# Kernel tuning notes

Measured on AMD Instinct MI355X. Metric: run time of the kernel, lower is better.

Reference implementation:

```python
import jax, jax.numpy as jnp
import numpy as np
from jax import lax

STRIDE = 4
SCALES = (32.0, 64.0, 128.0)
RATIOS = (0.5, 1.0, 2.0)
PRE_NMS = 6000          # pre_nms_top_n['testing']
POST_NMS = 1000         # post_nms_top_n['testing']
NMS_THRESH = 0.7
MIN_SIZE = 1.0


def make_anchors(fh, fw):
    # 9 base anchors per cell (3 scales x 3 ratios), xyxy centered at cell centers.
    base = []
    for s in SCALES:
        for r in RATIOS:
            w = s * np.sqrt(1.0 / r)
            h = s * np.sqrt(r)
            base.append([-w / 2, -h / 2, w / 2, h / 2])
    base = np.asarray(base, np.float32)                      # [9,4]
    xs = (np.arange(fw, dtype=np.float32) + 0.5) * STRIDE
    ys = (np.arange(fh, dtype=np.float32) + 0.5) * STRIDE
    cx, cy = np.meshgrid(xs, ys)                             # [fh,fw]
    shifts = np.stack([cx, cy, cx, cy], -1)[:, :, None, :]   # [fh,fw,1,4]
    return jnp.asarray((shifts + base[None, None]).reshape(-1, 4))  # [fh*fw*9,4]


def conv(x, w, b):
    y = lax.conv_general_dilated(x, w, (1, 1), 'SAME',
                                 dimension_numbers=('NCHW', 'OIHW', 'NCHW'))
    return y + b[None, :, None, None]


def decode(anchors, deltas):
    wa = anchors[:, 2] - anchors[:, 0]
    ha = anchors[:, 3] - anchors[:, 1]
    cxa = anchors[:, 0] + 0.5 * wa
    cya = anchors[:, 1] + 0.5 * ha
    cx = deltas[:, 0] * wa + cxa
    cy = deltas[:, 1] * ha + cya
    w = jnp.exp(deltas[:, 2]) * wa
    h = jnp.exp(deltas[:, 3]) * ha
    return jnp.stack([cx - 0.5 * w, cy - 0.5 * h, cx + 0.5 * w, cy + 0.5 * h], -1)


def pairwise_iou(a, b):
    area_a = (a[:, 2] - a[:, 0]) * (a[:, 3] - a[:, 1])
    area_b = (b[:, 2] - b[:, 0]) * (b[:, 3] - b[:, 1])
    lt = jnp.maximum(a[:, None, :2], b[None, :, :2])
    rb = jnp.minimum(a[:, None, 2:], b[None, :, 2:])
    wh = jnp.clip(rb - lt, 0.0)
    inter = wh[..., 0] * wh[..., 1]
    return inter / (area_a[:, None] + area_b[None, :] - inter + 1e-9)


def nms_keep(boxes, valid, thresh):
    # boxes already sorted by score descending; greedy suppression.
    n = boxes.shape[0]
    iou = pairwise_iou(boxes, boxes)  # [n,n]
    def body(i, keep):
        suppressed = jnp.any((iou[i] > thresh) & keep)
        return keep.at[i].set(valid[i] & ~suppressed)
    return lax.fori_loop(0, n, body, jnp.zeros(n, bool))


def rpn_forward(feature, w1, b1, w_cls, b_cls, w_reg, b_reg, image_h, image_w,
                detach_for_proposal=True):
    fh, fw = feature.shape[2], feature.shape[3]
    x = jax.nn.relu(conv(feature, w1, b1))
    conf = conv(x, w_cls, b_cls).transpose(0, 2, 3, 1).reshape(-1)        # [N]
    offsets = conv(x, w_reg, b_reg).transpose(0, 2, 3, 1).reshape(-1, 4)  # [N,4]
    if detach_for_proposal:  # original detaches before create_proposal
        conf = lax.stop_gradient(conf)
        offsets = lax.stop_gradient(offsets)
    anchors = make_anchors(fh, fw)

    pre_n = min(PRE_NMS, conf.shape[0])
    scores, idx = lax.top_k(conf, pre_n)
    props = decode(anchors[idx], offsets[idx])
    # process_box: clip to image, drop boxes smaller than min_size (mask form)
    props = jnp.stack([jnp.clip(props[:, 0], 0.0, float(image_w)),
                       jnp.clip(props[:, 1], 0.0, float(image_h)),
                       jnp.clip(props[:, 2], 0.0, float(image_w)),
                       jnp.clip(props[:, 3], 0.0, float(image_h))], -1)
    valid = ((props[:, 2] - props[:, 0]) >= MIN_SIZE) & \
            ((props[:, 3] - props[:, 1]) >= MIN_SIZE)

    keep = nms_keep(lax.stop_gradient(props), valid, NMS_THRESH)
    # compact first POST_NMS kept boxes into a fixed-shape output (zero padded)
    rank = jnp.cumsum(keep) - 1
    dest = jnp.where(keep & (rank < POST_NMS), rank, POST_NMS)
    out = jnp.zeros((POST_NMS + 1, 4), props.dtype).at[dest].set(props)[:POST_NMS]
    return out


def setup_inputs() -> dict:
    key = jax.random.key(0)
    ks = jax.random.split(key, 4)
    return {
        'feature': jax.random.normal(ks[0], (1, 256, 200, 272), jnp.float32),
        'w1': jax.random.normal(ks[1], (256, 256, 3, 3), jnp.float32) * 0.02,
        'b1': jnp.zeros((256,), jnp.float32),
        'w_cls': jax.random.normal(ks[2], (9, 256, 1, 1), jnp.float32) * 0.02,
        'b_cls': jnp.zeros((9,), jnp.float32),
        'w_reg': jax.random.normal(ks[3], (36, 256, 1, 1), jnp.float32) * 0.01,
        'b_reg': jnp.zeros((36,), jnp.float32),
        'image_h': 800,
        'image_w': 1088,
    }


def reference(feature, w1, b1, w_cls, b_cls, w_reg, b_reg, image_h, image_w):
    return rpn_forward(feature, w1, b1, w_cls, b_cls, w_reg, b_reg,
                       image_h, image_w, detach_for_proposal=True)
```

## Files before the change

kernel.cpp:

```cpp
#include <hip/hip_runtime.h>
#include <hip/hip_bf16.h>
#include <math.h>

#define H_ 200
#define W_ 272
#define C_ 256
#define HW 54400
#define NANCH 489600
#define PRE_N 6000
#define POST_N 1000
#define NWORDS 94
#define CHUNK_W 2720
#define SELCAP 16384

#define X_OFF       0ull
#define CONF_OFF    55705600ull
#define HIST1_OFF   57664000ull
#define SEL_OFF     57926144ull
#define SCAL_OFF    58188288ull
#define TOPIDX_OFF  58254080ull
#define BOXES_OFF   58278080ull
#define VALID_OFF   58374080ull
#define MASK_OFF    58398080ull
#define WCR_OFF     65269376ull

__device__ __forceinline__ unsigned fkey(float fv) {
    unsigned u = __float_as_uint(fv);
    return (u & 0x80000000u) ? ~u : (u | 0x80000000u);
}

__global__ __launch_bounds__(256) void k_repack(const float* __restrict__ w1,
                                                float* __restrict__ w1r) {
    int d = blockIdx.x * 256 + threadIdx.x;
    int o = d & 15;
    int q = d >> 4;
    int t = q % 9;
    int icg = q / 9;
    int wg16 = icg >> 8, ic = icg & 255;
    w1r[d] = w1[((size_t)(wg16 * 16 + o) * 256 + ic) * 9 + t];
}

__global__ __launch_bounds__(256) void k_conv1(const float* __restrict__ f,
                                               const float* __restrict__ w1r,
                                               const float* __restrict__ b1,
                                               float* __restrict__ xo,
                                               unsigned* __restrict__ hist1,
                                               unsigned* __restrict__ scal,
                                               unsigned long long* __restrict__ sel,
                                               const float* __restrict__ wcls,
                                               float* __restrict__ wcr) {
    __shared__ __align__(16) float sI[2][2880];
    int tid = threadIdx.x;
    int fb = blockIdx.x + 9 * (blockIdx.y + 25 * blockIdx.z);
    {
        int g = fb * 256 + tid;
        if (g < 65536) hist1[g] = 0u;
        else if (g < 65600) scal[g - 65536] = 0u;
        else if (g < 98368) ((unsigned*)sel)[g - 65600] = 0xFFFFFFFFu;
    }
    if (fb == 0) {
        for (int e = tid; e < 2304; e += 256) {
            int a = e / 256, c = e % 256;
            wcr[c * 9 + a] = wcls[e];
        }
    }
    int lane = tid & 63;
    int wgl = __builtin_amdgcn_readfirstlane(tid >> 6);
    int xg = lane & 7;
    int yg = lane >> 3;
    int X0 = blockIdx.x * 32;
    int Y0 = blockIdx.y * 8;
    int wg16 = blockIdx.z * 4 + wgl;
    int y = Y0 + yg;
    int xbase = X0 + xg * 4;

    int off[11]; int lds[11]; bool ok[11];
#pragma unroll
    for (int it = 0; it < 11; it++) {
        int l = tid + it * 256;
        int ci = l / 340; int r = l - ci * 340; int ry = r / 34; int rx = r - ry * 34;
        int gx = X0 - 1 + rx, gy = Y0 - 1 + ry;
        ok[it] = (l < CHUNK_W) && gx >= 0 && gx < W_ && gy >= 0 && gy < H_;
        off[it] = ci * HW + gy * W_ + gx;
        lds[it] = (ci * 10 + ry) * 36 + rx;
    }
    float rbuf[11];
#pragma unroll
    for (int it = 0; it < 11; it++)
        rbuf[it] = ok[it] ? f[off[it]] : 0.f;
#pragma unroll
    for (int it = 0; it < 11; it++)
        if (tid + it * 256 < CHUNK_W) sI[0][lds[it]] = rbuf[it];
    __syncthreads();

    float acc[16][4];
#pragma unroll
    for (int o = 0; o < 16; o++)
#pragma unroll
        for (int i = 0; i < 4; i++) acc[o][i] = 0.f;

    const float* wbase = w1r + (size_t)wg16 * (256 * 144);

    int cur = 0;
    for (int ic0 = 0; ic0 < 256; ic0 += 8) {
        if (ic0 < 248) {
            const float* fn = f + (size_t)(ic0 + 8) * HW;
#pragma unroll
            for (int it = 0; it < 11; it++)
                rbuf[it] = ok[it] ? fn[off[it]] : 0.f;
        }
        const float* sbuf = sI[cur];
        for (int ci = 0; ci < 8; ci++) {
            const float* wci = wbase + (ic0 + ci) * 144;
#pragma unroll
            for (int ky = 0; ky < 3; ky++) {
                const float* irow = &sbuf[(ci * 10 + yg + ky) * 36 + xg * 4];
                float4 va = *(const float4*)irow;
                float2 vb = *(const float2*)(irow + 4);
                float in[6] = {va.x, va.y, va.z, va.w, vb.x, vb.y};
#pragma unroll
                for (int kx = 0; kx < 3; kx++) {
                    const float* w16 = wci + (ky * 3 + kx) * 16;
#pragma unroll
                    for (int o = 0; o < 16; o++) {
                        float w = w16[o];
#pragma unroll
                        for (int i = 0; i < 4; i++)
                            acc[o][i] = fmaf(w, in[i + kx], acc[o][i]);
                    }
                }
            }
        }
        if (ic0 < 248) {
#pragma unroll
            for (int it = 0; it < 11; it++)
                if (tid + it * 256 < CHUNK_W) sI[cur ^ 1][lds[it]] = rbuf[it];
        }
        __syncthreads();
        cur ^= 1;
    }
#pragma unroll
    for (int o = 0; o < 16; o++) {
        int oc = wg16 * 16 + o;
        float bv = b1[oc];
        float* orow = xo + (size_t)oc * HW + y * W_ + xbase;
        float v0 = fmaxf(acc[o][0] + bv, 0.f), v1 = fmaxf(acc[o][1] + bv, 0.f);
        float v2 = fmaxf(acc[o][2] + bv, 0.f), v3 = fmaxf(acc[o][3] + bv, 0.f);
        if (xbase + 3 < W_) {
            *(float4*)orow = make_float4(v0, v1, v2, v3);
        } else {
            float vv[4] = {v0, v1, v2, v3};
            for (int i = 0; i < 4; i++)
                if (xbase + i < W_) orow[i] = vv[i];
        }
    }
}

__global__ __launch_bounds__(256) void k_cls(const float* __restrict__ x,
                                             const float* __restrict__ wcr,
                                             const float* __restrict__ bc,
                                             float* __restrict__ conf,
                                             unsigned* __restrict__ hist) {
    int p = blockIdx.x * 256 + threadIdx.x;
    if (p >= HW) return;
    float acc[9];
#pragma unroll
    for (int a = 0; a < 9; a++) acc[a] = 0.f;
    for (int c = 0; c < 256; c++) {
        float xv = x[c * HW + p];
        const float* wp = wcr + c * 9;
#pragma unroll
        for (int a = 0; a < 9; a++) acc[a] = fmaf(wp[a], xv, acc[a]);
    }
#pragma unroll
    for (int a = 0; a < 9; a++) {
        float v = acc[a] + bc[a];
        conf[p * 9 + a] = v;
        atomicAdd(&hist[fkey(v) >> 16], 1u);
    }
}

__global__ __launch_bounds__(1024) void k_scan(const unsigned* __restrict__ hist,
                                               unsigned* scal) {
    __shared__ unsigned ssum[1024];
    int t = threadIdx.x;
    int base = 65535 - t * 64;
    unsigned s = 0;
    {
        const uint4* hp = (const uint4*)(hist + (base - 63));
#pragma unroll
        for (int k = 0; k < 16; k++) { uint4 v = hp[k]; s += v.x + v.y + v.z + v.w; }
    }
    ssum[t] = s;
    __syncthreads();
    for (int off = 1; off < 1024; off <<= 1) {
        unsigned v = (t >= off) ? ssum[t - off] : 0u;
        __syncthreads();
        ssum[t] += v;
        __syncthreads();
    }
    unsigned incl = ssum[t], excl = incl - s;
    if (excl < 6000u && 6000u <= incl) {
        unsigned run = excl;
        bool found = false;
        for (int pass = 0; pass < 2 && !found; pass++) {
            unsigned c32[32];
#pragma unroll
            for (int j = 0; j < 32; j++) c32[j] = hist[base - (pass * 32 + j)];
            for (int j = 0; j < 32; j++) {
                if (run + c32[j] >= 6000u) {
                    scal[0] = (unsigned)(base - (pass * 32 + j));
                    scal[1] = run;
                    found = true;
                    break;
                }
                run += c32[j];
            }
        }
    }
}

__global__ __launch_bounds__(256) void k_gather(const float* __restrict__ conf,
                                                unsigned* scal, unsigned long long* sel) {
    int n = blockIdx.x * 256 + threadIdx.x;
    if (n >= NANCH) return;
    unsigned B1 = scal[0], cnt1 = scal[1];
    unsigned key = fkey(conf[n]);
    unsigned pre = key >> 16;
    if (pre < B1) return;
    unsigned long long kk = ((unsigned long long)(~key) << 32) | (unsigned)n;
    if (pre > B1) {
        unsigned pos = atomicAdd(&scal[4], 1u);
        sel[pos] = kk;
    } else {
        unsigned pos = cnt1 + atomicAdd(&scal[5], 1u);
        if (pos < SELCAP) sel[pos] = kk;
    }
}

__global__ __launch_bounds__(256) void k_rank(const unsigned* __restrict__ scal,
                                              const unsigned long long* __restrict__ sel,
                                              unsigned* __restrict__ topidx) {
    __shared__ unsigned long long tile[2048];
    unsigned filled = scal[1] + scal[5];
    if (filled > SELCAP) filled = SELCAP;
    int i = blockIdx.x * 256 + threadIdx.x;
    unsigned long long mykey = sel[i];
    int rank = 0;
    for (int t0 = 0; t0 < SELCAP; t0 += 2048) {
        if (t0 >= (int)filled) break;
        __syncthreads();
        for (int l = threadIdx.x; l < 2048; l += 256)
            tile[l] = sel[t0 + l];
        __syncthreads();
        for (int l = 0; l < 2048; l += 4) {
            ulonglong2 p = *(const ulonglong2*)&tile[l];
            ulonglong2 q = *(const ulonglong2*)&tile[l + 2];
            rank += (p.x < mykey) + (p.y < mykey) + (q.x < mykey) + (q.y < mykey);
        }
    }
    if (i < (int)filled && rank < PRE_N)
        topidx[rank] = (unsigned)(mykey & 0xFFFFFFFFull);
}

__global__ __launch_bounds__(64) void k_prop(const float* __restrict__ x,
                                             const float* __restrict__ wreg,
                                             const float* __restrict__ breg,
                                             const unsigned* __restrict__ topidx,
                                             const int* __restrict__ imh, const int* __restrict__ imw,
                                             float* __restrict__ boxes, int* __restrict__ valid) {
    int r = blockIdx.x;
    int lane = threadIdx.x;
    unsigned n = topidx[r];
    int a = (int)(n % 9u); int p = (int)(n / 9u);
    const float* wr = wreg + (4 * a) * 256;
    float s0 = 0, s1 = 0, s2 = 0, s3 = 0;
    for (int c = lane; c < 256; c += 64) {
        float xv = x[c * HW + p];
        s0 = fmaf(wr[c], xv, s0);
        s1 = fmaf(wr[256 + c], xv, s1);
        s2 = fmaf(wr[512 + c], xv, s2);
        s3 = fmaf(wr[768 + c], xv, s3);
    }
#pragma unroll
    for (int off = 32; off >= 1; off >>= 1) {
        s0 += __shfl_down(s0, off);
        s1 += __shfl_down(s1, off);
        s2 += __shfl_down(s2, off);
        s3 += __shfl_down(s3, off);
    }
    if (lane == 0) {
        float dx = s0 + breg[4 * a], dy = s1 + breg[4 * a + 1];
        float dw = s2 + breg[4 * a + 2], dh = s3 + breg[4 * a + 3];
        int wi = p % W_, hi = p / W_;
        const double SC[3] = {32.0, 64.0, 128.0};
        const double RT[3] = {0.5, 1.0, 2.0};
        double sd = SC[a / 3], rd = RT[a % 3];
        double wb = sd * sqrt(1.0 / rd), hb = sd * sqrt(rd);
        float bx1 = (float)(-wb * 0.5), by1 = (float)(-hb * 0.5);
        float bx2 = (float)(wb * 0.5),  by2 = (float)(hb * 0.5);
        float cxs = ((float)wi + 0.5f) * 4.0f, cys = ((float)hi + 0.5f) * 4.0f;
        float x1a = cxs + bx1, y1a = cys + by1, x2a = cxs + bx2, y2a = cys + by2;
        float wa = x2a - x1a, ha = y2a - y1a;
        float cxa = x1a + 0.5f * wa, cya = y1a + 0.5f * ha;
        float cx = dx * wa + cxa, cy = dy * ha + cya;
        float ww = expf(dw) * wa, hh = expf(dh) * ha;
        float X1 = cx - 0.5f * ww, Y1 = cy - 0.5f * hh;
        float X2 = cx + 0.5f * ww, Y2 = cy + 0.5f * hh;
        float Wf = (float)(*imw), Hf = (float)(*imh);
        X1 = fminf(fmaxf(X1, 0.f), Wf); Y1 = fminf(fmaxf(Y1, 0.f), Hf);
        X2 = fminf(fmaxf(X2, 0.f), Wf); Y2 = fminf(fmaxf(Y2, 0.f), Hf);
        boxes[4 * r] = X1; boxes[4 * r + 1] = Y1; boxes[4 * r + 2] = X2; boxes[4 * r + 3] = Y2;
        valid[r] = ((X2 - X1) >= 1.0f && (Y2 - Y1) >= 1.0f) ? 1 : 0;
    }
}

__global__ __launch_bounds__(256) void k_mask(const float* __restrict__ boxes,
                                              unsigned long long* __restrict__ mask) {
    __shared__ float jb[256];
    int jw = blockIdx.x;
    int i = blockIdx.y * 256 + threadIdx.x;
    {
        int idx = jw * 256 + threadIdx.x;
        jb[threadIdx.x] = (idx < PRE_N * 4) ? boxes[idx] : 0.f;
    }
    __syncthreads();
    if (i >= PRE_N) return;
    float ax1 = boxes[4 * i], ay1 = boxes[4 * i + 1], ax2 = boxes[4 * i + 2], ay2 = boxes[4 * i + 3];
    float aarea = (ax2 - ax1) * (ay2 - ay1);
    unsigned long long m = 0;
    int jbase = jw * 64;
    for (int b = 0; b < 64; b++) {
        int j = jbase + b;
        if (j <= i || j >= PRE_N) continue;
        float bx1 = jb[4 * b], by1 = jb[4 * b + 1], bx2 = jb[4 * b + 2], by2 = jb[4 * b + 3];
        float barea = (bx2 - bx1) * (by2 - by1);
        float xx1 = fmaxf(ax1, bx1), yy1 = fmaxf(ay1, by1);
        float xx2 = fminf(ax2, bx2), yy2 = fminf(ay2, by2);
        float w = fmaxf(xx2 - xx1, 0.f), h = fmaxf(yy2 - yy1, 0.f);
        float inter = w * h;
        float iou = inter / (aarea + barea - inter + 1e-9f);
        if (iou > 0.7f) m |= (1ull << b);
    }
    mask[(size_t)i * NWORDS + jw] = m;
}

__global__ __launch_bounds__(256) void k_scan_nms(const unsigned long long* __restrict__ mask,
                                                  const int* __restrict__ valid,
                                                  const float* __restrict__ boxes,
                                                  float* __restrict__ out) {
    __shared__ unsigned long long diag[NWORDS][64];
    __shared__ unsigned long long removed[NWORDS];
    __shared__ unsigned long long validw[NWORDS];
    __shared__ int keepList[POST_N];
    __shared__ int cnt;
    __shared__ unsigned long long keptbits;
    int t = threadIdx.x;
    if (t < NWORDS) { removed[t] = 0ull; validw[t] = 0ull; }
    if (t == 0) cnt = 0;
    __syncthreads();
    for (int l = t; l < NWORDS * 64; l += 256) {
        int w = l >> 6, b = l & 63;
        int i = w * 64 + b;
        diag[w][b] = (i < PRE_N) ? mask[(size_t)i * NWORDS + w] : 0ull;
    }
    for (int i = t; i < PRE_N; i += 256)
        if (valid[i]) atomicOr(&validw[i >> 6], 1ull << (i & 63));
    __syncthreads();
    for (int w = 0; w < NWORDS; w++) {
        unsigned long long candw = validw[w] & ~removed[w];
        if (!candw) continue;
        if (t < 64) {
            unsigned long long mydiag = diag[w][t];
            unsigned long long cand = candw;
            unsigned long long kb = 0ull;
            int c = cnt;
            while (cand && c < POST_N) {
                int b = __ffsll((unsigned long long)cand) - 1;
                unsigned long long sup = __shfl(mydiag, b);
                if (t == 0) keepList[c] = w * 64 + b;
                c++;
                kb |= 1ull << b;
                cand &= ~(1ull << b);
                cand &= ~sup;
            }
            if (t == 0) { cnt = c; keptbits = kb; }
        }
        __syncthreads();
        if (cnt >= POST_N) break;
        unsigned long long kb = keptbits;
        if (kb) {
            for (int w2 = w + 1 + t; w2 < NWORDS; w2 += 256) {
                unsigned long long acc2 = removed[w2];
                unsigned long long tt = kb;
                while (tt) {
                    int b = __ffsll((unsigned long long)tt) - 1;
                    tt &= tt - 1;
                    acc2 |= mask[(size_t)(w * 64 + b) * NWORDS + w2];
                }
                removed[w2] = acc2;
            }
        }
        __syncthreads();
    }
    __syncthreads();
    int c = cnt;
    for (int e = t; e < POST_N * 4; e += 256) {
        int r = e >> 2;
        out[e] = (r < c) ? boxes[4 * keepList[r] + (e & 3)] : 0.f;
    }
}

extern "C" void kernel_launch(void* const* d_in, const int* in_sizes, int n_in,
                              void* d_out, int out_size, void* d_ws, size_t ws_size,
                              hipStream_t stream) {
    const float* feature = (const float*)d_in[0];
    const float* w1   = (const float*)d_in[1];
    const float* b1   = (const float*)d_in[2];
    const float* wcls = (const float*)d_in[3];
    const float* bcls = (const float*)d_in[4];
    const float* wreg = (const float*)d_in[5];
    const float* breg = (const float*)d_in[6];
    const int* imh = (const int*)d_in[7];
    const int* imw = (const int*)d_in[8];

    char* ws = (char*)d_ws;
    float* xbuf  = (float*)(ws + X_OFF);
    float* conf  = (float*)(ws + CONF_OFF);
    unsigned* hist1 = (unsigned*)(ws + HIST1_OFF);
    unsigned* scal  = (unsigned*)(ws + SCAL_OFF);
    unsigned long long* sel = (unsigned long long*)(ws + SEL_OFF);
    unsigned* topidx = (unsigned*)(ws + TOPIDX_OFF);
    float* boxes = (float*)(ws + BOXES_OFF);
    int* valid   = (int*)(ws + VALID_OFF);
    unsigned long long* mask = (unsigned long long*)(ws + MASK_OFF);
    float* w1r = (float*)(ws + MASK_OFF);
    float* wcr = (float*)(ws + WCR_OFF);
    float* outF = (float*)d_out;

    hipLaunchKernelGGL(k_repack, dim3(2304), dim3(256), 0, stream, w1, w1r);
    hipLaunchKernelGGL(k_conv1,  dim3(9, 25, 4), dim3(256), 0, stream,
                       feature, w1r, b1, xbuf, hist1, scal, sel, wcls, wcr);
    hipLaunchKernelGGL(k_cls,    dim3(213),  dim3(256), 0, stream, xbuf, wcr, bcls, conf, hist1);
    hipLaunchKernelGGL(k_scan,   dim3(1),    dim3(1024), 0, stream, hist1, scal);
    hipLaunchKernelGGL(k_gather, dim3(1913), dim3(256), 0, stream, conf, scal, sel);
    hipLaunchKernelGGL(k_rank,   dim3(64),   dim3(256), 0, stream, scal, sel, topidx);
    hipLaunchKernelGGL(k_prop,   dim3(PRE_N), dim3(64), 0, stream, xbuf, wreg, breg, topidx, imh, imw, boxes, valid);
    hipLaunchKernelGGL(k_mask,   dim3(NWORDS, 24), dim3(256), 0, stream, boxes, mask);
    hipLaunchKernelGGL(k_scan_nms, dim3(1), dim3(256), 0, stream, mask, valid, boxes, outF);
}
```

Measured before the change: 1.667 ms.

## Use packed v_pk_fma_f32 in conv1 and halve per-wave output channels

Rewrites the 3x3 conv inner loop to use inline-asm v_pk_fma_f32. Each instruction applies two scalar-register weights to pairs of adjacent pixels, which is meant to halve the FMA instruction count. Each wave now computes 8 output channels instead of 16, with the weight repack and grid z-dimension adjusted to match. This lowers accumulator register pressure and doubles the block count, at the cost of twice as many input tile loads into LDS and fewer FMAs per LDS read.

```diff
diff --git a/kernel.cpp b/kernel.cpp
--- a/kernel.cpp
+++ b/kernel.cpp
@@ -24,6 +24,13 @@
 #define MASK_OFF    58398080ull
 #define WCR_OFF     65269376ull
 
+typedef float v2f __attribute__((ext_vector_type(2)));
+
+#define PKFMA_LO(d, a, wb) \
+    asm("v_pk_fma_f32 %0, %1, %2, %0 op_sel_hi:[1,0,1]" : "+v"(d) : "v"(a), "s"(wb))
+#define PKFMA_HI(d, a, wb) \
+    asm("v_pk_fma_f32 %0, %1, %2, %0 op_sel:[0,1,0] op_sel_hi:[1,1,1]" : "+v"(d) : "v"(a), "s"(wb))
+
 __device__ __forceinline__ unsigned fkey(float fv) {
     unsigned u = __float_as_uint(fv);
     return (u & 0x80000000u) ? ~u : (u | 0x80000000u);
@@ -32,12 +39,12 @@
 __global__ __launch_bounds__(256) void k_repack(const float* __restrict__ w1,
                                                 float* __restrict__ w1r) {
     int d = blockIdx.x * 256 + threadIdx.x;
-    int o = d & 15;
-    int q = d >> 4;
+    int o = d & 7;
+    int q = d >> 3;
     int t = q % 9;
     int icg = q / 9;
-    int wg16 = icg >> 8, ic = icg & 255;
-    w1r[d] = w1[((size_t)(wg16 * 16 + o) * 256 + ic) * 9 + t];
+    int wg8 = icg >> 8, ic = icg & 255;
+    w1r[d] = w1[((size_t)(wg8 * 8 + o) * 256 + ic) * 9 + t];
 }
 
 __global__ __launch_bounds__(256) void k_conv1(const float* __restrict__ f,
@@ -70,7 +77,7 @@
     int yg = lane >> 3;
     int X0 = blockIdx.x * 32;
     int Y0 = blockIdx.y * 8;
-    int wg16 = blockIdx.z * 4 + wgl;
+    int wg = blockIdx.z * 4 + wgl;
     int y = Y0 + yg;
     int xbase = X0 + xg * 4;
 
@@ -93,13 +100,14 @@
         if (tid + it * 256 < CHUNK_W) sI[0][lds[it]] = rbuf[it];
     __syncthreads();
 
-    float acc[16][4];
-#pragma unroll
-    for (int o = 0; o < 16; o++)
-#pragma unroll
-        for (int i = 0; i < 4; i++) acc[o][i] = 0.f;
-
-    const float* wbase = w1r + (size_t)wg16 * (256 * 144);
+    v2f acc2[8][2];
+#pragma unroll
+    for (int o = 0; o < 8; o++) {
+        acc2[o][0] = (v2f)(0.f);
+        acc2[o][1] = (v2f)(0.f);
+    }
+
+    const float* wbase = w1r + (size_t)wg * (256 * 72);
 
     int cur = 0;
     for (int ic0 = 0; ic0 < 256; ic0 += 8) {
@@ -111,7 +119,7 @@
         }
         const float* sbuf = sI[cur];
         for (int ci = 0; ci < 8; ci++) {
-            const float* wci = wbase + (ic0 + ci) * 144;
+            const float* wci = wbase + (ic0 + ci) * 72;
 #pragma unroll
             for (int ky = 0; ky < 3; ky++) {
                 const float* irow = &sbuf[(ci * 10 + yg + ky) * 36 + xg * 4];
@@ -120,13 +128,17 @@
                 float in[6] = {va.x, va.y, va.z, va.w, vb.x, vb.y};
 #pragma unroll
                 for (int kx = 0; kx < 3; kx++) {
-                    const float* w16 = wci + (ky * 3 + kx) * 16;
-#pragma unroll
-                    for (int o = 0; o < 16; o++) {
-                        float w = w16[o];
-#pragma unroll
-                        for (int i = 0; i < 4; i++)
-                            acc[o][i] = fmaf(w, in[i + kx], acc[o][i]);
+                    v2f q0; q0.x = in[kx];     q0.y = in[kx + 1];
+                    v2f q1; q1.x = in[kx + 2]; q1.y = in[kx + 3];
+                    const unsigned long long* wp =
+                        (const unsigned long long*)(wci + (ky * 3 + kx) * 8);
+#pragma unroll
+                    for (int o2 = 0; o2 < 4; o2++) {
+                        unsigned long long wb = wp[o2];
+                        PKFMA_LO(acc2[2 * o2][0], q0, wb);
+                        PKFMA_LO(acc2[2 * o2][1], q1, wb);
+                        PKFMA_HI(acc2[2 * o2 + 1][0], q0, wb);
+                        PKFMA_HI(acc2[2 * o2 + 1][1], q1, wb);
                     }
                 }
             }
@@ -140,12 +152,12 @@
         cur ^= 1;
     }
 #pragma unroll
-    for (int o = 0; o < 16; o++) {
-        int oc = wg16 * 16 + o;
+    for (int o = 0; o < 8; o++) {
+        int oc = wg * 8 + o;
         float bv = b1[oc];
         float* orow = xo + (size_t)oc * HW + y * W_ + xbase;
-        float v0 = fmaxf(acc[o][0] + bv, 0.f), v1 = fmaxf(acc[o][1] + bv, 0.f);
-        float v2 = fmaxf(acc[o][2] + bv, 0.f), v3 = fmaxf(acc[o][3] + bv, 0.f);
+        float v0 = fmaxf(acc2[o][0].x + bv, 0.f), v1 = fmaxf(acc2[o][0].y + bv, 0.f);
+        float v2 = fmaxf(acc2[o][1].x + bv, 0.f), v3 = fmaxf(acc2[o][1].y + bv, 0.f);
         if (xbase + 3 < W_) {
             *(float4*)orow = make_float4(v0, v1, v2, v3);
         } else {
@@ -439,7 +451,7 @@
     float* outF = (float*)d_out;
 
     hipLaunchKernelGGL(k_repack, dim3(2304), dim3(256), 0, stream, w1, w1r);
-    hipLaunchKernelGGL(k_conv1,  dim3(9, 25, 4), dim3(256), 0, stream,
+    hipLaunchKernelGGL(k_conv1,  dim3(9, 25, 8), dim3(256), 0, stream,
                        feature, w1r, b1, xbuf, hist1, scal, sel, wcls, wcr);
     hipLaunchKernelGGL(k_cls,    dim3(213),  dim3(256), 0, stream, xbuf, wcr, bcls, conf, hist1);
     hipLaunchKernelGGL(k_scan,   dim3(1),    dim3(1024), 0, stream, hist1, scal);
```

Result: no change. 1.646 ms (-1.3%).
